# Optimization experiments

Measured on AMD Instinct MI355X. Metric: run time of the kernel, lower is better.

Reference implementation:

```python
import jax, jax.numpy as jnp
import numpy as np

N = 100000      # nodes
E = 1600000     # edges (avg degree 16)
D_IN = 128
D_OUT = 128


def setup_inputs() -> dict:
    key = jax.random.key(0)
    k_x, k_e, k_w1, k_w2 = jax.random.split(key, 4)
    x = jax.random.normal(k_x, (N, D_IN), dtype=jnp.float32)
    edge_index = jax.random.randint(k_e, (2, E), 0, N, dtype=jnp.int64)
    # xavier_uniform for Linear weights, zero biases (as in reset_parameters)
    lim1 = float(np.sqrt(6.0 / (D_IN + D_OUT)))
    lim2 = float(np.sqrt(6.0 / (D_OUT + D_OUT)))
    W1 = jax.random.uniform(k_w1, (D_IN, D_OUT), jnp.float32, -lim1, lim1)
    b1 = jnp.zeros((D_OUT,), jnp.float32)
    W2 = jax.random.uniform(k_w2, (D_OUT, D_OUT), jnp.float32, -lim2, lim2)
    b2 = jnp.zeros((D_OUT,), jnp.float32)
    eps = jnp.zeros((1,), jnp.float32)  # trainable eps, init 0
    return {"x": x, "edge_index": edge_index, "W1": W1, "b1": b1,
            "W2": W2, "b2": b2, "eps": eps}


def reference(x, edge_index, W1, b1, W2, b2, eps):
    src, dst = edge_index[0], edge_index[1]
    # adj_t.matmul(x): agg[i] = sum_{j in N(i)} x[j]  (gather + scatter-add)
    agg = jax.ops.segment_sum(x[src], dst, num_segments=N)  # [N, D_IN]
    h = (1.0 + eps) * x + agg                                 # eps residual
    h = jax.nn.relu(h @ W1 + b1)                              # Linear + ReLU
    return h @ W2 + b2                                        # Linear
```

## Files before the change

### kernel.cpp

```cpp
#include <hip/hip_runtime.h>

#define DFEAT 128
#define NGRP 8
#define SSLOT 8
#define OVCAP 32768
#define FILL_BLOCKS 2048
#define EPT 8

typedef __attribute__((ext_vector_type(8))) short short8v;
typedef __attribute__((ext_vector_type(4))) float f32x4;
typedef __attribute__((ext_vector_type(4))) unsigned short ushort4v;

__device__ __forceinline__ unsigned short f2bf(float f) {
    union { float f; unsigned u; } cv; cv.f = f;
    unsigned u = cv.u + 0x7fffu + ((cv.u >> 16) & 1u);
    return (unsigned short)(u >> 16);
}
__device__ __forceinline__ float bf2f(unsigned short h) {
    union { unsigned u; float f; } cv; cv.u = ((unsigned)h) << 16; return cv.f;
}
__device__ __forceinline__ int load_idx(const void* eiv, int is64, size_t i) {
    return is64 ? (int)((const long long*)eiv)[i] : ((const int*)eiv)[i];
}

__global__ __launch_bounds__(256) void prep_kernel(
        const float* __restrict__ W1, const float* __restrict__ W2,
        unsigned short* __restrict__ w1bf, unsigned short* __restrict__ w2bf,
        const float* __restrict__ x, unsigned short* __restrict__ xb, int total4,
        const void* __restrict__ eiv,
        int* __restrict__ counts, int* __restrict__ ovcnt,
        int2* __restrict__ ov, int* __restrict__ slab,
        int E, int N, int nfill) {
    const int b = blockIdx.x;

    if (b < nfill) {
        const int* e32 = (const int*)eiv;
        int orsum = 0;
#pragma unroll
        for (int i = 0; i < 128; ++i) orsum |= e32[2 * i + 1];
        const int is64 = (orsum == 0);

        const int gtid = b * 256 + threadIdx.x;
        const int stride = nfill * 256;
        const int grp = b & (NGRP - 1);

        int sr[EPT], ds[EPT];
        int k = 0;
        for (int e = gtid; e < E && k < EPT; e += stride) {
            sr[k] = load_idx(eiv, is64, (size_t)e);
            ds[k] = load_idx(eiv, is64, (size_t)E + e);
            ++k;
        }

        const int sz = (N + NGRP - 1) / NGRP;
        for (int s = 0; s < NGRP; ++s) {
            int lo = s * sz, hi = lo + sz;
#pragma unroll
            for (int i = 0; i < EPT; ++i) {
                if (i < k && ds[i] >= lo && ds[i] < hi) {
                    int pos = atomicAdd(&counts[(size_t)grp * N + ds[i]], 1);
                    if (pos < SSLOT)
                        slab[((size_t)grp * N + ds[i]) * SSLOT + pos] = sr[i];
                    else {
                        int o = atomicAdd(ovcnt, 1);
                        if (o < OVCAP) ov[o] = make_int2(ds[i], sr[i]);
                    }
                }
            }
        }
    } else if (b < nfill + 128) {
        int wb = b - nfill;
        const float* W = (wb < 64) ? W1 : W2;
        unsigned short* o = (wb < 64) ? w1bf : w2bf;
        int idx = (wb & 63) * 256 + threadIdx.x;
        int kk = idx >> 7, n = idx & 127;
        o[n * 128 + kk] = f2bf(W[idx]);
    } else {
        int i = (b - nfill - 128) * 256 + threadIdx.x;
        if (i < total4) {
            float4 v = *(const float4*)&x[(size_t)i * 4];
            ushort4v o;
            o.x = f2bf(v.x); o.y = f2bf(v.y); o.z = f2bf(v.z); o.w = f2bf(v.w);
            *(ushort4v*)&xb[(size_t)i * 4] = o;
        }
    }
}

__global__ __launch_bounds__(256) void agg_slab_kernel(
        const unsigned short* __restrict__ xb,
        const int* __restrict__ counts,
        const int* __restrict__ slab,
        const int* __restrict__ ovcnt, const int2* __restrict__ ov,
        const float* __restrict__ epsp,
        unsigned short* __restrict__ hb,
        float* __restrict__ hf,
        int N) {
    __shared__ int comp[8][64];
    const int lane = threadIdx.x & 31;
    const int grpq = threadIdx.x >> 5;
    const int base = threadIdx.x & 32;
    const int node = blockIdx.x * 8 + grpq;
    if (node >= N) return;
    const int c = lane * 4;
    const float epsv = 1.0f + epsp[0];

    int g = lane >> 2, s0 = (lane & 3) * 2;
    int2 sl = *(const int2*)&slab[((size_t)g * N + node) * SSLOT + s0];
    int cnt = min(counts[(size_t)g * N + node], SSLOT);
    bool v0 = s0 < cnt, v1 = (s0 + 1) < cnt;
    unsigned m0 = (unsigned)(__ballot(v0) >> base);
    unsigned m1 = (unsigned)(__ballot(v1) >> base);
    int t0 = __popc(m0);
    int total = t0 + __popc(m1);
    unsigned lt = (lane == 0) ? 0u : (~0u >> (32 - lane));
    if (v0) comp[grpq][__popc(m0 & lt)] = sl.x;
    if (v1) comp[grpq][t0 + __popc(m1 & lt)] = sl.y;

    ushort4v own = *(const ushort4v*)&xb[(size_t)node * DFEAT + c];
    float ax = epsv * bf2f(own.x), ay = epsv * bf2f(own.y);
    float az = epsv * bf2f(own.z), aw = epsv * bf2f(own.w);

    for (int i = 0; i < total; i += 16) {
        int4 q0 = *(const int4*)&comp[grpq][i];
        int4 q1 = *(const int4*)&comp[grpq][i + 4];
        int4 q2 = *(const int4*)&comp[grpq][i + 8];
        int4 q3 = *(const int4*)&comp[grpq][i + 12];
        int rem = total - i;
        int sj[16];
        sj[0]  = q0.x;
        sj[1]  = (rem > 1)  ? q0.y : q0.x;
        sj[2]  = (rem > 2)  ? q0.z : q0.x;
        sj[3]  = (rem > 3)  ? q0.w : q0.x;
        sj[4]  = (rem > 4)  ? q1.x : q0.x;
        sj[5]  = (rem > 5)  ? q1.y : q0.x;
        sj[6]  = (rem > 6)  ? q1.z : q0.x;
        sj[7]  = (rem > 7)  ? q1.w : q0.x;
        sj[8]  = (rem > 8)  ? q2.x : q0.x;
        sj[9]  = (rem > 9)  ? q2.y : q0.x;
        sj[10] = (rem > 10) ? q2.z : q0.x;
        sj[11] = (rem > 11) ? q2.w : q0.x;
        sj[12] = (rem > 12) ? q3.x : q0.x;
        sj[13] = (rem > 13) ? q3.y : q0.x;
        sj[14] = (rem > 14) ? q3.z : q0.x;
        sj[15] = (rem > 15) ? q3.w : q0.x;
        ushort4v u[16];
#pragma unroll
        for (int q = 0; q < 16; ++q)
            u[q] = *(const ushort4v*)&xb[(size_t)sj[q] * DFEAT + c];
#pragma unroll
        for (int q = 0; q < 16; ++q) {
            if (rem > q) {
                ax += bf2f(u[q].x); ay += bf2f(u[q].y);
                az += bf2f(u[q].z); aw += bf2f(u[q].w);
            }
        }
    }

    int ovn = min(ovcnt[0], OVCAP);
    int trips = (ovn + 31) >> 5;
    for (int t = 0; t < trips; ++t) {
        int j = t * 32 + lane;
        int2 e = (j < ovn) ? ov[j] : make_int2(-1, 0);
        unsigned long long b = __ballot(e.x == node);
        unsigned m = (unsigned)(b >> base);
        while (m) {
            int l = __ffs(m) - 1; m &= m - 1;
            int s = __shfl(e.y, base + l, 64);
            ushort4v u = *(const ushort4v*)&xb[(size_t)s * DFEAT + c];
            ax += bf2f(u.x); ay += bf2f(u.y);
            az += bf2f(u.z); aw += bf2f(u.w);
        }
    }

    if (hb) {
        ushort4v hv;
        hv.x = f2bf(ax); hv.y = f2bf(ay); hv.z = f2bf(az); hv.w = f2bf(aw);
        *(ushort4v*)&hb[(size_t)node * DFEAT + c] = hv;
    } else {
        *(float4*)&hf[(size_t)node * DFEAT + c] = make_float4(ax, ay, az, aw);
    }
}

__global__ __launch_bounds__(256) void mlp_mfma_kernel(
        const unsigned short* __restrict__ hb,
        const float* __restrict__ hsrc,
        const unsigned short* __restrict__ w1bf,
        const unsigned short* __restrict__ w2bf,
        const float* __restrict__ b1, const float* __restrict__ b2,
        float* __restrict__ out, int N) {
    __shared__ unsigned short hlds[64 * 136];
    __shared__ unsigned short wlds[128 * 136];

    const int tid  = threadIdx.x;
    const int node0 = blockIdx.x * 64;
    const int lane = tid & 63;
    const int w    = tid >> 6;
    const int l15  = lane & 15;
    const int quad = lane >> 4;

    if (hb) {
        for (int i = tid; i < 64 * 16; i += 256) {
            int m = i >> 4, k0 = (i & 15) * 8;
            int node = node0 + m;
            short8v v = {0, 0, 0, 0, 0, 0, 0, 0};
            if (node < N) v = *(const short8v*)&hb[(size_t)node * DFEAT + k0];
            *(short8v*)&hlds[m * 136 + k0] = v;
        }
    } else {
        for (int i = tid; i < 64 * 32; i += 256) {
            int m = i >> 5, c = (i & 31) * 4;
            int node = node0 + m;
            float4 v = make_float4(0.f, 0.f, 0.f, 0.f);
            if (node < N) v = *(const float4*)&hsrc[(size_t)node * DFEAT + c];
            ushort4v o;
            o.x = f2bf(v.x); o.y = f2bf(v.y); o.z = f2bf(v.z); o.w = f2bf(v.w);
            *(ushort4v*)&hlds[m * 136 + c] = o;
        }
    }
    for (int i = tid; i < 128 * 16; i += 256) {
        int n = i >> 4, k0 = (i & 15) * 8;
        *(short8v*)&wlds[n * 136 + k0] = *(const short8v*)&w1bf[n * 128 + k0];
    }
    __syncthreads();

    const unsigned short* ha = &hlds[(w * 16 + l15) * 136 + quad * 8];

    for (int layer = 0; layer < 2; ++layer) {
        if (layer == 1) {
            __syncthreads();
            for (int i = tid; i < 128 * 16; i += 256) {
                int n = i >> 4, k0 = (i & 15) * 8;
                *(short8v*)&wlds[n * 136 + k0] = *(const short8v*)&w2bf[n * 128 + k0];
            }
            __syncthreads();
        }

        f32x4 acc[8];
#pragma unroll
        for (int nt = 0; nt < 8; ++nt) acc[nt] = (f32x4){0.f, 0.f, 0.f, 0.f};

#pragma unroll
        for (int s = 0; s < 4; ++s) {
            short8v a = *(const short8v*)&ha[s * 32];
#pragma unroll
            for (int nt = 0; nt < 8; ++nt) {
                short8v bf = *(const short8v*)&wlds[(nt * 16 + l15) * 136 + quad * 8 + s * 32];
                acc[nt] = __builtin_amdgcn_mfma_f32_16x16x32_bf16(a, bf, acc[nt], 0, 0, 0);
            }
        }

        const float* bias = layer ? b2 : b1;
        if (layer == 0) {
            __syncthreads();
#pragma unroll
            for (int nt = 0; nt < 8; ++nt) {
                float bv = bias[nt * 16 + l15];
#pragma unroll
                for (int r = 0; r < 4; ++r) {
                    float v = fmaxf(acc[nt][r] + bv, 0.f);
                    hlds[(w * 16 + quad * 4 + r) * 136 + nt * 16 + l15] = f2bf(v);
                }
            }
        } else {
#pragma unroll
            for (int nt = 0; nt < 8; ++nt) {
                float bv = bias[nt * 16 + l15];
#pragma unroll
                for (int r = 0; r < 4; ++r) {
                    int node = node0 + w * 16 + quad * 4 + r;
                    if (node < N)
                        out[(size_t)node * DFEAT + nt * 16 + l15] = acc[nt][r] + bv;
                }
            }
        }
    }
}

__global__ void detect_idx_kernel(const int* __restrict__ ei, int* __restrict__ flag) {
    if (threadIdx.x == 0 && blockIdx.x == 0) {
        int orsum = 0;
#pragma unroll
        for (int i = 0; i < 128; ++i) orsum |= ei[2 * i + 1];
        flag[0] = (orsum == 0) ? 1 : 0;
    }
}

__global__ __launch_bounds__(256) void scatter_kernel(
        const float* __restrict__ x, const void* __restrict__ eiv,
        const int* __restrict__ flag, float* __restrict__ agg, int E) {
    unsigned gid = blockIdx.x * 256u + threadIdx.x;
    unsigned e = gid >> 5;
    if (e >= (unsigned)E) return;
    int c = (gid & 31u) * 4;
    int is64 = flag[0];
    int src = load_idx(eiv, is64, (size_t)e);
    int dst = load_idx(eiv, is64, (size_t)E + e);
    float4 v = *(const float4*)&x[(size_t)src * DFEAT + c];
    float* p = &agg[(size_t)dst * DFEAT + c];
    unsafeAtomicAdd(p + 0, v.x);
    unsafeAtomicAdd(p + 1, v.y);
    unsafeAtomicAdd(p + 2, v.z);
    unsafeAtomicAdd(p + 3, v.w);
}

__global__ __launch_bounds__(256) void mlp_kernel(
        const float* __restrict__ xp,
        const float* __restrict__ W1, const float* __restrict__ b1,
        const float* __restrict__ W2, const float* __restrict__ b2,
        const float* __restrict__ epsp, float* __restrict__ out) {
    __shared__ float hs[32][DFEAT];
    __shared__ float Wc[64][DFEAT];

    const int tid = threadIdx.x;
    const int node0 = blockIdx.x * 32;
    const float epsv = 1.0f + epsp[0];

    for (int i = tid; i < 32 * (DFEAT / 4); i += 256) {
        int n = i >> 5;
        int c = (i & 31) * 4;
        size_t off = (size_t)(node0 + n) * DFEAT + c;
        float4 h = *(const float4*)&out[off];
        float4 xv = *(const float4*)&xp[off];
        h.x += epsv * xv.x; h.y += epsv * xv.y;
        h.z += epsv * xv.z; h.w += epsv * xv.w;
        *(float4*)&hs[n][c] = h;
    }

    const int og = (tid & 31) * 4;
    const int ng = (tid >> 5) * 4;

    for (int layer = 0; layer < 2; ++layer) {
        const float* W = layer ? W2 : W1;
        const float* b = layer ? b2 : b1;

        float acc[4][4];
#pragma unroll
        for (int j = 0; j < 4; ++j) {
            float bj = b[og + j];
#pragma unroll
            for (int i = 0; i < 4; ++i) acc[i][j] = bj;
        }

        for (int chunk = 0; chunk < 2; ++chunk) {
            __syncthreads();
            for (int i = tid; i < 64 * (DFEAT / 4); i += 256) {
                int r = i >> 5;
                int c = (i & 31) * 4;
                *(float4*)&Wc[r][c] =
                    *(const float4*)&W[(size_t)(chunk * 64 + r) * DFEAT + c];
            }
            __syncthreads();
            const int kb = chunk * 64;
            for (int k = 0; k < 64; k += 4) {
                float4 h4[4], w4[4];
#pragma unroll
                for (int i = 0; i < 4; ++i)
                    h4[i] = *(const float4*)&hs[ng + i][kb + k];
#pragma unroll
                for (int j = 0; j < 4; ++j)
                    w4[j] = *(const float4*)&Wc[k + j][og];
#pragma unroll
                for (int i = 0; i < 4; ++i) {
                    acc[i][0] += h4[i].x * w4[0].x + h4[i].y * w4[1].x
                               + h4[i].z * w4[2].x + h4[i].w * w4[3].x;
                    acc[i][1] += h4[i].x * w4[0].y + h4[i].y * w4[1].y
                               + h4[i].z * w4[2].y + h4[i].w * w4[3].y;
                    acc[i][2] += h4[i].x * w4[0].z + h4[i].y * w4[1].z
                               + h4[i].z * w4[2].z + h4[i].w * w4[3].z;
                    acc[i][3] += h4[i].x * w4[0].w + h4[i].y * w4[1].w
                               + h4[i].z * w4[2].w + h4[i].w * w4[3].w;
                }
            }
        }
        __syncthreads();

        if (layer == 0) {
#pragma unroll
            for (int i = 0; i < 4; ++i) {
                float4 r;
                r.x = fmaxf(acc[i][0], 0.0f);
                r.y = fmaxf(acc[i][1], 0.0f);
                r.z = fmaxf(acc[i][2], 0.0f);
                r.w = fmaxf(acc[i][3], 0.0f);
                *(float4*)&hs[ng + i][og] = r;
            }
        } else {
#pragma unroll
            for (int i = 0; i < 4; ++i) {
                float4 r;
                r.x = acc[i][0]; r.y = acc[i][1];
                r.z = acc[i][2]; r.w = acc[i][3];
                *(float4*)&out[(size_t)(node0 + ng + i) * DFEAT + og] = r;
            }
        }
    }
}

extern "C" void kernel_launch(void* const* d_in, const int* in_sizes, int n_in,
                              void* d_out, int out_size, void* d_ws, size_t ws_size,
                              hipStream_t stream) {
    const float* x   = (const float*)d_in[0];
    const void*  ei  = d_in[1];
    const float* W1  = (const float*)d_in[2];
    const float* b1  = (const float*)d_in[3];
    const float* W2  = (const float*)d_in[4];
    const float* b2  = (const float*)d_in[5];
    const float* eps = (const float*)d_in[6];
    float* out = (float*)d_out;

    const int N = in_sizes[0] / DFEAT;
    const int E = in_sizes[1] / 2;
    const int M = NGRP * N;
    const int total4 = N * (DFEAT / 4);

    char* p = (char*)d_ws;
    unsigned short* w1bf = (unsigned short*)p;  p += 128 * 128 * 2;
    unsigned short* w2bf = (unsigned short*)p;  p += 128 * 128 * 2;
    unsigned short* xb = (unsigned short*)p;    p += (size_t)N * DFEAT * 2;
    int* counts = (int*)p;                      p += (size_t)M * 4;
    int* ovcnt = (int*)p;                       p += 64;
    int2* ov = (int2*)p;                        p += (size_t)OVCAP * 8;
    int* slab = (int*)p;                        p += (size_t)M * SSLOT * 4;
    size_t need_slim = (size_t)(p - (char*)d_ws);
    unsigned short* hb = (unsigned short*)p;    p += (size_t)N * DFEAT * 2;
    size_t need_full = (size_t)(p - (char*)d_ws);

    if (ws_size >= need_slim) {
        bool full = (ws_size >= need_full);
        int nfill = FILL_BLOCKS;
        if ((size_t)E > (size_t)FILL_BLOCKS * 256 * EPT)
            nfill = (E + 256 * EPT - 1) / (256 * EPT);
        int xbBlocks = (total4 + 255) / 256;

        hipMemsetAsync(counts, 0, (size_t)M * 4 + 64, stream);
        prep_kernel<<<nfill + 128 + xbBlocks, 256, 0, stream>>>(
            W1, W2, w1bf, w2bf, x, xb, total4, ei,
            counts, ovcnt, ov, slab, E, N, nfill);
        agg_slab_kernel<<<(N + 7) / 8, 256, 0, stream>>>(
            xb, counts, slab, ovcnt, ov, eps,
            full ? hb : nullptr, out, N);
        mlp_mfma_kernel<<<(N + 63) / 64, 256, 0, stream>>>(
            full ? hb : nullptr, out, w1bf, w2bf, b1, b2, out, N);
        return;
    }

    int* flag3 = (int*)d_ws;
    detect_idx_kernel<<<1, 64, 0, stream>>>((const int*)ei, flag3);
    hipMemsetAsync(d_out, 0, (size_t)out_size * sizeof(float), stream);
    unsigned total = (unsigned)E * 32u;
    scatter_kernel<<<(total + 255u) / 256u, 256, 0, stream>>>(x, ei, flag3, out, E);
    mlp_kernel<<<N / 32, 256, 0, stream>>>(x, W1, b1, W2, b2, eps, out);
}
```

Measured before the change: 291.8 us.

## Replace 8-group sharded slab with single per-node 32-slot adjacency slab

Removes the 8-way grouping of per-node counters and slabs and uses one counter and a 32-slot slab per destination node. The memset and workspace shrink from 8N counters and 64N slots to N counters and 32N slots. The aggregation kernel can now load the neighbor list with one coalesced read instead of a ballot/popcount compaction across groups. The trade-off is that all atomics for a node now hit one counter, which raises contention during the fill.

```diff
diff --git a/kernel.cpp b/kernel.cpp
--- a/kernel.cpp
+++ b/kernel.cpp
@@ -1,8 +1,8 @@
 #include <hip/hip_runtime.h>
 
 #define DFEAT 128
-#define NGRP 8
-#define SSLOT 8
+#define SSLOT 32
+#define NSWEEP 8
 #define OVCAP 32768
 #define FILL_BLOCKS 2048
 #define EPT 8
@@ -42,7 +42,6 @@
 
         const int gtid = b * 256 + threadIdx.x;
         const int stride = nfill * 256;
-        const int grp = b & (NGRP - 1);
 
         int sr[EPT], ds[EPT];
         int k = 0;
@@ -52,15 +51,15 @@
             ++k;
         }
 
-        const int sz = (N + NGRP - 1) / NGRP;
-        for (int s = 0; s < NGRP; ++s) {
+        const int sz = (N + NSWEEP - 1) / NSWEEP;
+        for (int s = 0; s < NSWEEP; ++s) {
             int lo = s * sz, hi = lo + sz;
 #pragma unroll
             for (int i = 0; i < EPT; ++i) {
                 if (i < k && ds[i] >= lo && ds[i] < hi) {
-                    int pos = atomicAdd(&counts[(size_t)grp * N + ds[i]], 1);
+                    int pos = atomicAdd(&counts[ds[i]], 1);
                     if (pos < SSLOT)
-                        slab[((size_t)grp * N + ds[i]) * SSLOT + pos] = sr[i];
+                        slab[(size_t)ds[i] * SSLOT + pos] = sr[i];
                     else {
                         int o = atomicAdd(ovcnt, 1);
                         if (o < OVCAP) ov[o] = make_int2(ds[i], sr[i]);
@@ -95,7 +94,7 @@
         unsigned short* __restrict__ hb,
         float* __restrict__ hf,
         int N) {
-    __shared__ int comp[8][64];
+    __shared__ int comp[8][SSLOT];
     const int lane = threadIdx.x & 31;
     const int grpq = threadIdx.x >> 5;
     const int base = threadIdx.x & 32;
@@ -104,17 +103,8 @@
     const int c = lane * 4;
     const float epsv = 1.0f + epsp[0];
 
-    int g = lane >> 2, s0 = (lane & 3) * 2;
-    int2 sl = *(const int2*)&slab[((size_t)g * N + node) * SSLOT + s0];
-    int cnt = min(counts[(size_t)g * N + node], SSLOT);
-    bool v0 = s0 < cnt, v1 = (s0 + 1) < cnt;
-    unsigned m0 = (unsigned)(__ballot(v0) >> base);
-    unsigned m1 = (unsigned)(__ballot(v1) >> base);
-    int t0 = __popc(m0);
-    int total = t0 + __popc(m1);
-    unsigned lt = (lane == 0) ? 0u : (~0u >> (32 - lane));
-    if (v0) comp[grpq][__popc(m0 & lt)] = sl.x;
-    if (v1) comp[grpq][t0 + __popc(m1 & lt)] = sl.y;
+    const int total = min(counts[node], SSLOT);
+    if (lane < total) comp[grpq][lane] = slab[(size_t)node * SSLOT + lane];
 
     ushort4v own = *(const ushort4v*)&xb[(size_t)node * DFEAT + c];
     float ax = epsv * bf2f(own.x), ay = epsv * bf2f(own.y);
@@ -161,8 +151,8 @@
     for (int t = 0; t < trips; ++t) {
         int j = t * 32 + lane;
         int2 e = (j < ovn) ? ov[j] : make_int2(-1, 0);
-        unsigned long long b = __ballot(e.x == node);
-        unsigned m = (unsigned)(b >> base);
+        unsigned long long bm = __ballot(e.x == node);
+        unsigned m = (unsigned)(bm >> base);
         while (m) {
             int l = __ffs(m) - 1; m &= m - 1;
             int s = __shfl(e.y, base + l, 64);
@@ -410,17 +400,16 @@
 
     const int N = in_sizes[0] / DFEAT;
     const int E = in_sizes[1] / 2;
-    const int M = NGRP * N;
     const int total4 = N * (DFEAT / 4);
 
     char* p = (char*)d_ws;
     unsigned short* w1bf = (unsigned short*)p;  p += 128 * 128 * 2;
     unsigned short* w2bf = (unsigned short*)p;  p += 128 * 128 * 2;
     unsigned short* xb = (unsigned short*)p;    p += (size_t)N * DFEAT * 2;
-    int* counts = (int*)p;                      p += (size_t)M * 4;
+    int* counts = (int*)p;                      p += (size_t)N * 4;
     int* ovcnt = (int*)p;                       p += 64;
     int2* ov = (int2*)p;                        p += (size_t)OVCAP * 8;
-    int* slab = (int*)p;                        p += (size_t)M * SSLOT * 4;
+    int* slab = (int*)p;                        p += (size_t)N * SSLOT * 4;
     size_t need_slim = (size_t)(p - (char*)d_ws);
     unsigned short* hb = (unsigned short*)p;    p += (size_t)N * DFEAT * 2;
     size_t need_full = (size_t)(p - (char*)d_ws);
@@ -432,7 +421,7 @@
             nfill = (E + 256 * EPT - 1) / (256 * EPT);
         int xbBlocks = (total4 + 255) / 256;
 
-        hipMemsetAsync(counts, 0, (size_t)M * 4 + 64, stream);
+        hipMemsetAsync(counts, 0, (size_t)N * 4 + 64, stream);
         prep_kernel<<<nfill + 128 + xbBlocks, 256, 0, stream>>>(
             W1, W2, w1bf, w2bf, x, xb, total4, ei,
             counts, ovcnt, ov, slab, E, N, nfill);
```

Result: slower. 331.5 us (+13.6%).

## Embed per-node counts in slab rows and bucket the overflow list by node range

Applied to the files above, without the earlier changes.

Each slab row grows to 8 words: word 0 holds the atomic count and seven neighbor slots follow, replacing the separate counts array. The aggregation kernel then fetches count and indices in one load and recovers the count with a shuffle. The single global overflow list becomes 64 buckets keyed by dst>>11, so each node scans only its own bucket instead of every overflow entry. In exchange the memset now has to zero the whole slab, and dropping to 7 slots per row pushes more edges into overflow.

```diff
diff --git a/kernel.cpp b/kernel.cpp
--- a/kernel.cpp
+++ b/kernel.cpp
@@ -2,8 +2,10 @@
 
 #define DFEAT 128
 #define NGRP 8
-#define SSLOT 8
-#define OVCAP 32768
+#define SWORDS 8
+#define SSLOT 7
+#define OVBKT 64
+#define OVCAPB 1024
 #define FILL_BLOCKS 2048
 #define EPT 8
 
@@ -28,8 +30,8 @@
         unsigned short* __restrict__ w1bf, unsigned short* __restrict__ w2bf,
         const float* __restrict__ x, unsigned short* __restrict__ xb, int total4,
         const void* __restrict__ eiv,
-        int* __restrict__ counts, int* __restrict__ ovcnt,
-        int2* __restrict__ ov, int* __restrict__ slab,
+        int* __restrict__ ovcnt, int2* __restrict__ ov,
+        int* __restrict__ slab,
         int E, int N, int nfill) {
     const int b = blockIdx.x;
 
@@ -58,12 +60,14 @@
 #pragma unroll
             for (int i = 0; i < EPT; ++i) {
                 if (i < k && ds[i] >= lo && ds[i] < hi) {
-                    int pos = atomicAdd(&counts[(size_t)grp * N + ds[i]], 1);
+                    size_t sbase = ((size_t)grp * N + ds[i]) * SWORDS;
+                    int pos = atomicAdd(&slab[sbase], 1);
                     if (pos < SSLOT)
-                        slab[((size_t)grp * N + ds[i]) * SSLOT + pos] = sr[i];
+                        slab[sbase + 1 + pos] = sr[i];
                     else {
-                        int o = atomicAdd(ovcnt, 1);
-                        if (o < OVCAP) ov[o] = make_int2(ds[i], sr[i]);
+                        int bkt = ds[i] >> 11;
+                        int o = atomicAdd(&ovcnt[bkt], 1);
+                        if (o < OVCAPB) ov[bkt * OVCAPB + o] = make_int2(ds[i], sr[i]);
                     }
                 }
             }
@@ -88,7 +92,6 @@
 
 __global__ __launch_bounds__(256) void agg_slab_kernel(
         const unsigned short* __restrict__ xb,
-        const int* __restrict__ counts,
         const int* __restrict__ slab,
         const int* __restrict__ ovcnt, const int2* __restrict__ ov,
         const float* __restrict__ epsp,
@@ -104,10 +107,13 @@
     const int c = lane * 4;
     const float epsv = 1.0f + epsp[0];
 
-    int g = lane >> 2, s0 = (lane & 3) * 2;
-    int2 sl = *(const int2*)&slab[((size_t)g * N + node) * SSLOT + s0];
-    int cnt = min(counts[(size_t)g * N + node], SSLOT);
-    bool v0 = s0 < cnt, v1 = (s0 + 1) < cnt;
+    int g = lane >> 2, p = lane & 3;
+    int2 sl = *(const int2*)&slab[((size_t)g * N + node) * SWORDS + 2 * p];
+    int craw = __shfl(sl.x, base + (g << 2), 64);
+    int cnt = min(craw, SSLOT);
+    int w0 = 2 * p, w1 = 2 * p + 1;
+    bool v0 = (w0 >= 1) && (w0 <= cnt);
+    bool v1 = (w1 <= cnt);
     unsigned m0 = (unsigned)(__ballot(v0) >> base);
     unsigned m1 = (unsigned)(__ballot(v1) >> base);
     int t0 = __popc(m0);
@@ -156,19 +162,23 @@
         }
     }
 
-    int ovn = min(ovcnt[0], OVCAP);
-    int trips = (ovn + 31) >> 5;
-    for (int t = 0; t < trips; ++t) {
-        int j = t * 32 + lane;
-        int2 e = (j < ovn) ? ov[j] : make_int2(-1, 0);
-        unsigned long long b = __ballot(e.x == node);
-        unsigned m = (unsigned)(b >> base);
-        while (m) {
-            int l = __ffs(m) - 1; m &= m - 1;
-            int s = __shfl(e.y, base + l, 64);
-            ushort4v u = *(const ushort4v*)&xb[(size_t)s * DFEAT + c];
-            ax += bf2f(u.x); ay += bf2f(u.y);
-            az += bf2f(u.z); aw += bf2f(u.w);
+    {
+        const int bkt = node >> 11;
+        const int2* ovb = &ov[(size_t)bkt * OVCAPB];
+        int ovn = min(ovcnt[bkt], OVCAPB);
+        int trips = (ovn + 31) >> 5;
+        for (int t = 0; t < trips; ++t) {
+            int j = t * 32 + lane;
+            int2 e = (j < ovn) ? ovb[j] : make_int2(-1, 0);
+            unsigned long long bm = __ballot(e.x == node);
+            unsigned m = (unsigned)(bm >> base);
+            while (m) {
+                int l = __ffs(m) - 1; m &= m - 1;
+                int s = __shfl(e.y, base + l, 64);
+                ushort4v u = *(const ushort4v*)&xb[(size_t)s * DFEAT + c];
+                ax += bf2f(u.x); ay += bf2f(u.y);
+                az += bf2f(u.z); aw += bf2f(u.w);
+            }
         }
     }
 
@@ -417,10 +427,9 @@
     unsigned short* w1bf = (unsigned short*)p;  p += 128 * 128 * 2;
     unsigned short* w2bf = (unsigned short*)p;  p += 128 * 128 * 2;
     unsigned short* xb = (unsigned short*)p;    p += (size_t)N * DFEAT * 2;
-    int* counts = (int*)p;                      p += (size_t)M * 4;
-    int* ovcnt = (int*)p;                       p += 64;
-    int2* ov = (int2*)p;                        p += (size_t)OVCAP * 8;
-    int* slab = (int*)p;                        p += (size_t)M * SSLOT * 4;
+    int2* ov = (int2*)p;                        p += (size_t)OVBKT * OVCAPB * 8;
+    int* ovcnt = (int*)p;                       p += 1024;
+    int* slab = (int*)p;                        p += (size_t)M * SWORDS * 4;
     size_t need_slim = (size_t)(p - (char*)d_ws);
     unsigned short* hb = (unsigned short*)p;    p += (size_t)N * DFEAT * 2;
     size_t need_full = (size_t)(p - (char*)d_ws);
@@ -432,12 +441,12 @@
             nfill = (E + 256 * EPT - 1) / (256 * EPT);
         int xbBlocks = (total4 + 255) / 256;
 
-        hipMemsetAsync(counts, 0, (size_t)M * 4 + 64, stream);
+        hipMemsetAsync(ovcnt, 0, 1024 + (size_t)M * SWORDS * 4, stream);
         prep_kernel<<<nfill + 128 + xbBlocks, 256, 0, stream>>>(
             W1, W2, w1bf, w2bf, x, xb, total4, ei,
-            counts, ovcnt, ov, slab, E, N, nfill);
+            ovcnt, ov, slab, E, N, nfill);
         agg_slab_kernel<<<(N + 7) / 8, 256, 0, stream>>>(
-            xb, counts, slab, ovcnt, ov, eps,
+            xb, slab, ovcnt, ov, eps,
             full ? hb : nullptr, out, N);
         mlp_mfma_kernel<<<(N + 63) / 64, 256, 0, stream>>>(
             full ? hb : nullptr, out, w1bf, w2bf, b1, b2, out, N);
```

Measured after the change: 369.5 us. 26.6% more time.
